# Optimization experiments

Hardware: AMD Instinct MI355X
Metric: run time of the kernel (lower is better)

## Reference

```python
import jax, jax.numpy as jnp
import numpy as np

H = 60.0  # self.h
C = jnp.array([10665991.0, 27000000.0, 7953253.0], dtype=jnp.float32)  # self.c (9e6*3 = 27e6)


def setup_inputs() -> dict:
    key = jax.random.key(0)
    k1, k2, k3 = jax.random.split(key, 3)
    B, T = 8192, 1024
    # room temperatures in Kelvin, strictly positive (model uses 1/x)
    x0 = 280.0 + 20.0 * jax.random.uniform(k1, (B, 3), dtype=jnp.float32)
    u = jax.random.uniform(k2, (B, T, 8), dtype=jnp.float32)
    # col 0: external temperature ~[250,300] K; cols 1..7: positive power/irradiation
    u = u.at[:, :, 0].set(250.0 + 50.0 * u[:, :, 0])
    u = u.at[:, :, 1:].multiply(1000.0)
    # 14 scalar log-conductance params: [l12, l23, le1..3, ls1..3, lh1..3, lc1..3]
    lam = 0.1 * jax.random.normal(k3, (14,), dtype=jnp.float32)
    return {"x0": x0, "u": u, "lam": lam}


def _forward(x0, u, lam):
    e = jnp.exp(lam)
    e12, e23 = e[0], e[1]
    ee, es, eh, ec = e[2:5], e[5:8], e[8:11], e[11:14]  # each [3]

    def step(x, ut):  # x: [B,3], ut: [B,8]
        inv = 1.0 / x
        d12 = inv[:, 0] - inv[:, 1]
        d23 = inv[:, 1] - inv[:, 2]
        # A @ x^T, with A's only nonzeros at (0,1),(1,0),(1,2),(2,1)
        Ax = jnp.stack([
            e12 * d12 * x[:, 1],
            -e12 * d12 * x[:, 0] + e23 * d23 * x[:, 2],
            -e23 * d23 * x[:, 1],
        ], axis=-1)  # [B,3]
        u0 = ut[:, 0:1]  # external temperature
        # B @ u_t: external exchange + solar + per-room heating (u2..4) + cooling (u5..7)
        Bu = (ee * (inv - 1.0 / u0) * u0
              + es * ut[:, 1:2]
              + eh * ut[:, 2:5]
              + ec * ut[:, 5:8])  # [B,3]
        x_new = x * jnp.exp(H * (Ax + Bu) / C)
        return x_new, x_new

    # loop runs for T-1 steps using u[:, t] for t = 0..T-2
    u_seq = jnp.swapaxes(u[:, :-1, :], 0, 1)  # [T-1, B, 8]
    _, xs = jax.lax.scan(step, x0, u_seq)
    preds_rest = jnp.swapaxes(xs, 0, 1)  # [B, T-1, 3]
    # rows where the NEXT step's external temp is ~0 are flagged with -1
    invalid = u[:, 1:, 0] < 1e-6  # [B, T-1]
    preds_rest = jnp.where(invalid[..., None], jnp.float32(-1.0), preds_rest)
    return jnp.concatenate([x0[:, None, :], preds_rest], axis=1)  # [B, T, 3]


def reference(x0, u, lam):
    return _forward(x0, u, lam)
```

## Files before the change

kernel.cpp:

```cpp
#include <hip/hip_runtime.h>


#if __has_builtin(__builtin_amdgcn_exp2f)
#define EXP2F(x) __builtin_amdgcn_exp2f(x)
#else
#define EXP2F(x) __expf((x) * 0.69314718056f)
#endif

namespace {
constexpr int T = 1024;
constexpr int NBLK = T / 8;
constexpr float LOG2E = 1.4426950408889634f;
constexpr int CH_STRIDE = 68;
}

__device__ __forceinline__ float rfl(float x) {
    return __int_as_float(__builtin_amdgcn_readfirstlane(__float_as_int(x)));
}

__global__ __launch_bounds__(256, 1) void bm_fwd(
    const float* __restrict__ x0p,
    const float* __restrict__ up,
    const float* __restrict__ lamp,
    float* __restrict__ outp)
{
    __shared__ float lds[32 * CH_STRIDE];

    const int tid   = blockIdx.x * 256 + threadIdx.x;
    const int chain = tid >> 3;
    const int phase = tid & 7;
    const int g     = (threadIdx.x >> 3) & 7;
    float* __restrict__ region = lds + (threadIdx.x >> 3) * CH_STRIDE;
    float* __restrict__ wslot  = region + ((phase ^ g) << 3);

    float e[14];
#pragma unroll
    for (int i = 0; i < 14; ++i) e[i] = expf(lamp[i]);

    const float hc0 = (60.0f / 10665991.0f) * LOG2E;
    const float hc1 = (60.0f / 27000000.0f) * LOG2E;
    const float hc2 = (60.0f / 7953253.0f) * LOG2E;
    const float F12_0 = rfl(hc0 * e[0]), F12_1 = rfl(hc1 * e[0]);
    const float F23_1 = rfl(hc1 * e[1]), F23_2 = rfl(hc2 * e[1]);
    const float hce0 = rfl(hc0 * e[2]),  hce1 = rfl(hc1 * e[3]),  hce2 = rfl(hc2 * e[4]);
    const float ss0  = rfl(hc0 * e[5]),  ss1  = rfl(hc1 * e[6]),  ss2  = rfl(hc2 * e[7]);
    const float sh0  = rfl(hc0 * e[8]),  sh1  = rfl(hc1 * e[9]),  sh2  = rfl(hc2 * e[10]);
    const float sc0  = rfl(hc0 * e[11]), sc1  = rfl(hc1 * e[12]), sc2  = rfl(hc2 * e[13]);
    const float g0c = rfl(-hce0 - F12_0);
    const float g1c = rfl(-hce1 - F12_1 - F23_1);
    const float g2c = rfl(-hce2 - F23_2);

    float X0 = x0p[3 * chain + 0];
    float X1 = x0p[3 * chain + 1];
    float X2 = x0p[3 * chain + 2];

    const float4* __restrict__ ub = (const float4*)(up + (size_t)chain * (T * 8));
    float* __restrict__ ob = outp + (size_t)chain * (T * 3);

    auto fold_write = [&](const float4& r0, const float4& r1) -> float {
        const float G0 = fmaf(sc0, r1.y, fmaf(sh0, r0.z, fmaf(ss0, r0.y, g0c)));
        const float G1 = fmaf(sc1, r1.z, fmaf(sh1, r0.w, fmaf(ss1, r0.y, g1c)));
        const float G2 = fmaf(sc2, r1.w, fmaf(sh2, r1.x, fmaf(ss2, r0.y, g2c)));
        *(float4*)wslot = make_float4(r0.x, G0, G1, G2);
        return r0.x;
    };

    auto issue_reads = [&](float4 (&A)[8]) {
#pragma unroll
        for (int i = 0; i < 8; ++i) {
            A[i] = *(float4*)(region + ((i ^ g) << 3));
        }
    };

    auto compute = [&](int j, const float4 (&A)[8], float myu0) {
        float O0 = 0.0f, O1 = 0.0f, O2 = 0.0f;
#pragma unroll
        for (int i = 0; i < 8; ++i) {
            if (phase == i) { O0 = X0; O1 = X1; O2 = X2; }
            const float u0b = A[i].x;
            const float E0 = hce0 * u0b;
            const float E1 = hce1 * u0b;
            const float E2 = hce2 * u0b;
            const float i0 = __builtin_amdgcn_rcpf(X0);
            const float i1 = __builtin_amdgcn_rcpf(X1);
            const float i2 = __builtin_amdgcn_rcpf(X2);
            const float p0 = fmaf(F12_0, X1, E0);
            const float p1 = fmaf(F12_1, X0, fmaf(F23_1, X2, E1));
            const float p2 = fmaf(F23_2, X1, E2);
            const float z0 = fmaf(i0, p0, A[i].y);
            const float z1 = fmaf(i1, p1, A[i].z);
            const float z2 = fmaf(i2, p2, A[i].w);
            X0 *= EXP2F(z0);
            X1 *= EXP2F(z1);
            X2 *= EXP2F(z2);
        }
        const bool bad = (myu0 < 1e-6f) && !((j == 0) & (phase == 0));
        float3 o;
        o.x = bad ? -1.0f : O0;
        o.y = bad ? -1.0f : O1;
        o.z = bad ? -1.0f : O2;
        *(float3*)(ob + (size_t)((j << 3) + phase) * 3) = o;
    };

    float4 setA[8], setB[8];
    float4 rE0, rE1, rO0, rO1;
    float myu0A, myu0B;

    {
        const float4* s0 = ub + (size_t)((0 + phase) * 2);
        float4 t0 = s0[0], t1 = s0[1];
        const float4* s1 = ub + (size_t)((8 + phase) * 2);
        rE0 = s1[0]; rE1 = s1[1];
        const float4* s2 = ub + (size_t)((16 + phase) * 2);
        rO0 = s2[0]; rO1 = s2[1];
        myu0A = fold_write(t0, t1);
        issue_reads(setA);
        __builtin_amdgcn_sched_barrier(0);
    }

    for (int j = 0; j < NBLK; j += 2) {
        myu0B = fold_write(rE0, rE1);
        {
            const int jj = (j + 3 < NBLK) ? (j + 3) : (NBLK - 1);
            const float4* s = ub + (size_t)(((jj << 3) + phase) * 2);
            rE0 = s[0]; rE1 = s[1];
        }
        issue_reads(setB);
        __builtin_amdgcn_sched_barrier(0);
        compute(j, setA, myu0A);

        myu0A = fold_write(rO0, rO1);
        {
            const int jj = (j + 4 < NBLK) ? (j + 4) : (NBLK - 1);
            const float4* s = ub + (size_t)(((jj << 3) + phase) * 2);
            rO0 = s[0]; rO1 = s[1];
        }
        issue_reads(setA);
        __builtin_amdgcn_sched_barrier(0);
        compute(j + 1, setB, myu0B);
    }
}

extern "C" void kernel_launch(void* const* d_in, const int* in_sizes, int n_in,
                              void* d_out, int out_size, void* d_ws, size_t ws_size,
                              hipStream_t stream) {
    const float* x0  = (const float*)d_in[0];
    const float* u   = (const float*)d_in[1];
    const float* lam = (const float*)d_in[2];
    float* out = (float*)d_out;

    const int B = in_sizes[0] / 3;
    const int threads = B * 8;
    dim3 grid(threads / 256), block(256);
    hipLaunchKernelGGL(bm_fwd, grid, block, 0, stream, x0, u, lam, out);
}
```

Measured before the change: 457.5 us.

## Use 16 lanes per chain with double-buffered LDS superblocks

Each recurrence chain is now handled by 16 lanes instead of 8. Every lane loads and folds one timestep of inputs into a double-buffered LDS region, and all 16 lanes redundantly step the recurrence through the superblock. The explicit register-prefetched LDS read sets, XOR-swizzling and sched barriers are removed in favour of direct per-step LDS reads, and launch bounds now allow 2 blocks per CU. This doubles the thread count and halves the number of outer iterations, at the cost of twice as much redundant serial compute per chain and LDS reads on the dependent chain.

```diff
diff --git a/kernel.cpp b/kernel.cpp
--- a/kernel.cpp
+++ b/kernel.cpp
@@ -9,29 +9,28 @@
 
 namespace {
 constexpr int T = 1024;
-constexpr int NBLK = T / 8;
+constexpr int SB = 16;
+constexpr int NSB = T / SB;
 constexpr float LOG2E = 1.4426950408889634f;
-constexpr int CH_STRIDE = 68;
+constexpr int CH_STRIDE = 132;
 }
 
 __device__ __forceinline__ float rfl(float x) {
     return __int_as_float(__builtin_amdgcn_readfirstlane(__float_as_int(x)));
 }
 
-__global__ __launch_bounds__(256, 1) void bm_fwd(
+__global__ __launch_bounds__(256, 2) void bm_fwd(
     const float* __restrict__ x0p,
     const float* __restrict__ up,
     const float* __restrict__ lamp,
     float* __restrict__ outp)
 {
-    __shared__ float lds[32 * CH_STRIDE];
+    __shared__ float lds[16 * CH_STRIDE];
 
     const int tid   = blockIdx.x * 256 + threadIdx.x;
-    const int chain = tid >> 3;
-    const int phase = tid & 7;
-    const int g     = (threadIdx.x >> 3) & 7;
-    float* __restrict__ region = lds + (threadIdx.x >> 3) * CH_STRIDE;
-    float* __restrict__ wslot  = region + ((phase ^ g) << 3);
+    const int chain = tid >> 4;
+    const int l     = tid & 15;
+    float* __restrict__ region = lds + (threadIdx.x >> 4) * CH_STRIDE;
 
     float e[14];
 #pragma unroll
@@ -57,87 +56,68 @@
     const float4* __restrict__ ub = (const float4*)(up + (size_t)chain * (T * 8));
     float* __restrict__ ob = outp + (size_t)chain * (T * 3);
 
-    auto fold_write = [&](const float4& r0, const float4& r1) -> float {
+    auto fold_write = [&](int par, const float4& r0, const float4& r1) -> float {
         const float G0 = fmaf(sc0, r1.y, fmaf(sh0, r0.z, fmaf(ss0, r0.y, g0c)));
         const float G1 = fmaf(sc1, r1.z, fmaf(sh1, r0.w, fmaf(ss1, r0.y, g1c)));
         const float G2 = fmaf(sc2, r1.w, fmaf(sh2, r1.x, fmaf(ss2, r0.y, g2c)));
-        *(float4*)wslot = make_float4(r0.x, G0, G1, G2);
+        *(float4*)(region + par * 64 + (l << 2)) = make_float4(r0.x, G0, G1, G2);
         return r0.x;
     };
 
-    auto issue_reads = [&](float4 (&A)[8]) {
+    float4 pf0, pf1;
+    float u0_cur;
+
+    {
+        const float4* s = ub + (size_t)(l * 2);
+        float4 t0 = s[0], t1 = s[1];
+        u0_cur = fold_write(0, t0, t1);
+        const float4* p = ub + (size_t)((SB + l) * 2);
+        pf0 = p[0]; pf1 = p[1];
+    }
+
+    for (int sb = 0; sb < NSB; ++sb) {
+        const int par = sb & 1;
+
+        const float u0_next = fold_write(par ^ 1, pf0, pf1);
+
+        {
+            const int jj = (sb + 2 < NSB) ? (sb + 2) : (NSB - 1);
+            const float4* p = ub + (size_t)((jj * SB + l) * 2);
+            pf0 = p[0]; pf1 = p[1];
+        }
+
+        float O0 = 0.0f, O1 = 0.0f, O2 = 0.0f;
+        const float* rdbase = region + par * 64;
 #pragma unroll
-        for (int i = 0; i < 8; ++i) {
-            A[i] = *(float4*)(region + ((i ^ g) << 3));
-        }
-    };
-
-    auto compute = [&](int j, const float4 (&A)[8], float myu0) {
-        float O0 = 0.0f, O1 = 0.0f, O2 = 0.0f;
-#pragma unroll
-        for (int i = 0; i < 8; ++i) {
-            if (phase == i) { O0 = X0; O1 = X1; O2 = X2; }
-            const float u0b = A[i].x;
-            const float E0 = hce0 * u0b;
-            const float E1 = hce1 * u0b;
-            const float E2 = hce2 * u0b;
+        for (int i = 0; i < SB; ++i) {
+            const float4 r = *(const float4*)(rdbase + (i << 2));
+            if (l == i) { O0 = X0; O1 = X1; O2 = X2; }
             const float i0 = __builtin_amdgcn_rcpf(X0);
             const float i1 = __builtin_amdgcn_rcpf(X1);
             const float i2 = __builtin_amdgcn_rcpf(X2);
+            const float E0 = hce0 * r.x;
+            const float E1 = hce1 * r.x;
+            const float E2 = hce2 * r.x;
             const float p0 = fmaf(F12_0, X1, E0);
             const float p1 = fmaf(F12_1, X0, fmaf(F23_1, X2, E1));
             const float p2 = fmaf(F23_2, X1, E2);
-            const float z0 = fmaf(i0, p0, A[i].y);
-            const float z1 = fmaf(i1, p1, A[i].z);
-            const float z2 = fmaf(i2, p2, A[i].w);
+            const float z0 = fmaf(i0, p0, r.y);
+            const float z1 = fmaf(i1, p1, r.z);
+            const float z2 = fmaf(i2, p2, r.w);
             X0 *= EXP2F(z0);
             X1 *= EXP2F(z1);
             X2 *= EXP2F(z2);
         }
-        const bool bad = (myu0 < 1e-6f) && !((j == 0) & (phase == 0));
+
+        const int t = sb * SB + l;
+        const bool bad = (u0_cur < 1e-6f) && (t != 0);
         float3 o;
         o.x = bad ? -1.0f : O0;
         o.y = bad ? -1.0f : O1;
         o.z = bad ? -1.0f : O2;
-        *(float3*)(ob + (size_t)((j << 3) + phase) * 3) = o;
-    };
+        *(float3*)(ob + (size_t)t * 3) = o;
 
-    float4 setA[8], setB[8];
-    float4 rE0, rE1, rO0, rO1;
-    float myu0A, myu0B;
-
-    {
-        const float4* s0 = ub + (size_t)((0 + phase) * 2);
-        float4 t0 = s0[0], t1 = s0[1];
-        const float4* s1 = ub + (size_t)((8 + phase) * 2);
-        rE0 = s1[0]; rE1 = s1[1];
-        const float4* s2 = ub + (size_t)((16 + phase) * 2);
-        rO0 = s2[0]; rO1 = s2[1];
-        myu0A = fold_write(t0, t1);
-        issue_reads(setA);
-        __builtin_amdgcn_sched_barrier(0);
-    }
-
-    for (int j = 0; j < NBLK; j += 2) {
-        myu0B = fold_write(rE0, rE1);
-        {
-            const int jj = (j + 3 < NBLK) ? (j + 3) : (NBLK - 1);
-            const float4* s = ub + (size_t)(((jj << 3) + phase) * 2);
-            rE0 = s[0]; rE1 = s[1];
-        }
-        issue_reads(setB);
-        __builtin_amdgcn_sched_barrier(0);
-        compute(j, setA, myu0A);
-
-        myu0A = fold_write(rO0, rO1);
-        {
-            const int jj = (j + 4 < NBLK) ? (j + 4) : (NBLK - 1);
-            const float4* s = ub + (size_t)(((jj << 3) + phase) * 2);
-            rO0 = s[0]; rO1 = s[1];
-        }
-        issue_reads(setA);
-        __builtin_amdgcn_sched_barrier(0);
-        compute(j + 1, setB, myu0B);
+        u0_cur = u0_next;
     }
 }
 
@@ -150,7 +130,7 @@
     float* out = (float*)d_out;
 
     const int B = in_sizes[0] / 3;
-    const int threads = B * 8;
+    const int threads = B * 16;
     dim3 grid(threads / 256), block(256);
     hipLaunchKernelGGL(bm_fwd, grid, block, 0, stream, x0, u, lam, out);
 }
```

Measured after the change: 436.0 us. 4.7% less time.
